# Kernel optimization log

Hardware: AMD Instinct MI355X
Metric: run time of the kernel (lower is better)

The kernel has to match this reference:

```python
import jax, jax.numpy as jnp
import numpy as np

B, S, D = 2, 2048, 2048
H = 16
DR = 64      # qk_rope_head_dim
DN = 64      # qk_nope_head_dim
DQK = DN + DR
DV = 128     # v_head_dim
QLR = 1536   # q_lora_rank
KVLR = 1024  # kv_lora_rank
THETA = 10000.0


def setup_inputs() -> dict:
    key = jax.random.key(0)
    ks = jax.random.split(key, 8)
    init = lambda k, shape: (jax.random.normal(k, shape, jnp.float32) * 0.02)
    x = jax.random.normal(ks[0], (B, S, D), jnp.float32)
    wq_a = init(ks[1], (QLR, D))
    q_norm_w = jnp.ones((QLR,), jnp.float32)
    wq_b = init(ks[2], (H * DQK, QLR))
    wkv_a = init(ks[3], (KVLR + DR, D))
    kv_norm_w = jnp.ones((KVLR,), jnp.float32)
    wkv_b = init(ks[4], (H * (DN + DV), KVLR))
    wo = init(ks[5], (D, H * DV))
    # rotary frequencies: angle[t, i] = t / theta^(2i/DR)  (complex freqs_cis = cos + i sin)
    inv_freq = 1.0 / (THETA ** (jnp.arange(0, DR, 2, dtype=jnp.float32) / DR))
    ang = jnp.arange(S, dtype=jnp.float32)[:, None] * inv_freq[None, :]  # [S, DR/2]
    freqs_cos, freqs_sin = jnp.cos(ang), jnp.sin(ang)
    # causal additive mask (large negative instead of -inf for grad safety)
    mask = jnp.where(jnp.triu(jnp.ones((S, S), bool), 1), -1e9, 0.0).astype(jnp.float32)
    return dict(x=x, wq_a=wq_a, q_norm_w=q_norm_w, wq_b=wq_b, wkv_a=wkv_a,
                kv_norm_w=kv_norm_w, wkv_b=wkv_b, wo=wo, mask=mask,
                freqs_cos=freqs_cos, freqs_sin=freqs_sin, start_pos=0)


def _rmsnorm(x, w, eps=1e-6):
    return x * jax.lax.rsqrt(jnp.mean(x * x, axis=-1, keepdims=True) + eps) * w


def _rope(x, cos, sin):
    # x: [B, S, h, d]; complex multiply on interleaved (even, odd) pairs
    x0, x1 = x[..., ::2], x[..., 1::2]
    c = cos[None, :, None, :]
    s = sin[None, :, None, :]
    return jnp.stack([x0 * c - x1 * s, x0 * s + x1 * c], axis=-1).reshape(x.shape)


def reference(x, wq_a, q_norm_w, wq_b, wkv_a, kv_norm_w, wkv_b, wo,
              mask, freqs_cos, freqs_sin, start_pos):
    # start_pos == 0 prefill: KV cache[:end_pos] equals current K/V.
    scale = DQK ** -0.5
    # low-rank Q: wq_b(q_norm(wq_a(x)))
    q = _rmsnorm(x @ wq_a.T, q_norm_w) @ wq_b.T
    q = q.reshape(B, S, H, DQK)
    q_nope, q_pe = q[..., :DN], q[..., DN:]
    q_pe = _rope(q_pe, freqs_cos, freqs_sin)
    # latent KV
    kv = x @ wkv_a.T                              # [B, S, KVLR + DR]
    c_kv, k_pe = kv[..., :KVLR], kv[..., KVLR:]
    k_pe = _rope(k_pe[:, :, None, :], freqs_cos, freqs_sin)   # [B, S, 1, DR]
    kv2 = (_rmsnorm(c_kv, kv_norm_w) @ wkv_b.T).reshape(B, S, H, DN + DV)
    k_nope, v = kv2[..., :DN], kv2[..., DN:]
    k = jnp.concatenate([k_nope, jnp.broadcast_to(k_pe, (B, S, H, DR))], axis=-1)
    qf = jnp.concatenate([q_nope, q_pe], axis=-1)             # [B, S, H, DQK]
    # scores laid out [B, S(q), H, T(k)] as in the torch code
    scores = jnp.einsum('bshd,bthd->bsht', qf, k) * scale + mask[None, :, None, :]
    attn = jax.nn.softmax(scores.astype(jnp.float32), axis=-1).astype(x.dtype)
    out = jnp.einsum('bsht,bthd->bshd', attn, v)              # [B, S, H, DV]
    return out.reshape(B, S, H * DV) @ wo.T
```

## Files before the change

kernel.cpp:

```cpp
#include <hip/hip_runtime.h>
#include <hip/hip_bf16.h>


using bf16 = __hip_bfloat16;
typedef __attribute__((ext_vector_type(8))) short bf16x8;
typedef __attribute__((ext_vector_type(4))) float f32x4;

#define S_ 2048
#define NEG_BIG (-1e30f)
#define LOG2E 1.4426950408889634f

static __device__ __forceinline__ f32x4 mfma16(bf16x8 a, bf16x8 b, f32x4 c) {
    return __builtin_amdgcn_mfma_f32_16x16x32_bf16(a, b, c, 0, 0, 0);
}

static __device__ __forceinline__ void gload_lds16(const bf16* g, bf16* l) {
    __builtin_amdgcn_global_load_lds(
        (const __attribute__((address_space(1))) void*)g,
        (__attribute__((address_space(3))) void*)l, 16, 0, 0);
}

__global__ __launch_bounds__(256) void f2b(const float* __restrict__ src,
                                           bf16* __restrict__ dst, int n4) {
    int i = blockIdx.x * 256 + threadIdx.x;
    if (i < n4) {
        float4 v = ((const float4*)src)[i];
        alignas(8) bf16 t[4];
        t[0] = (bf16)v.x; t[1] = (bf16)v.y; t[2] = (bf16)v.z; t[3] = (bf16)v.w;
        ((uint2*)dst)[i] = *(const uint2*)t;
    }
}

template <bool C_F32>
__global__ __launch_bounds__(256) void gemm_bt(const bf16* __restrict__ A,
                                               const bf16* __restrict__ Bw,
                                               void* __restrict__ Cv,
                                               int M, int N, int K,
                                               int lda, int ldb, int ldc) {
    __shared__ bf16 As[128 * 32];
    __shared__ bf16 Bs[128 * 32];
    const int tid = threadIdx.x;
    const int m0 = blockIdx.x * 128;
    const int n0 = blockIdx.y * 128;
    const int w = tid >> 6, lane = tid & 63, quad = lane >> 4, l15 = lane & 15;
    const int wr = (w >> 1) * 64, wc = (w & 1) * 64;

    f32x4 acc[4][4];
#pragma unroll
    for (int i = 0; i < 4; i++)
#pragma unroll
        for (int j = 0; j < 4; j++) acc[i][j] = (f32x4){0.f, 0.f, 0.f, 0.f};

    for (int k0 = 0; k0 < K; k0 += 32) {
        __syncthreads();
#pragma unroll
        for (int cc = 0; cc < 2; cc++) {
            int c = tid + cc * 256;
            int row = c >> 2;
            int chunk = (c & 3) ^ ((row >> 1) & 3);
            gload_lds16(A + (size_t)(m0 + row) * lda + k0 + chunk * 8, As + c * 8);
            gload_lds16(Bw + (size_t)(n0 + row) * ldb + k0 + chunk * 8, Bs + c * 8);
        }
        __syncthreads();
        bf16x8 af[4], bfr[4];
#pragma unroll
        for (int mi = 0; mi < 4; mi++) {
            int row = wr + mi * 16 + l15;
            int chunkE = quad ^ ((row >> 1) & 3);
            af[mi] = *(const bf16x8*)(&As[row * 32 + chunkE * 8]);
        }
#pragma unroll
        for (int ni = 0; ni < 4; ni++) {
            int row = wc + ni * 16 + l15;
            int chunkE = quad ^ ((row >> 1) & 3);
            bfr[ni] = *(const bf16x8*)(&Bs[row * 32 + chunkE * 8]);
        }
#pragma unroll
        for (int mi = 0; mi < 4; mi++)
#pragma unroll
            for (int ni = 0; ni < 4; ni++)
                acc[mi][ni] = mfma16(af[mi], bfr[ni], acc[mi][ni]);
    }

#pragma unroll
    for (int mi = 0; mi < 4; mi++) {
#pragma unroll
        for (int ni = 0; ni < 4; ni++) {
            int col = n0 + wc + ni * 16 + l15;
            if (col < N) {
#pragma unroll
                for (int r = 0; r < 4; r++) {
                    int row = m0 + wr + mi * 16 + quad * 4 + r;
                    if (C_F32) ((float*)Cv)[(size_t)row * ldc + col] = acc[mi][ni][r];
                    else       ((bf16*)Cv)[(size_t)row * ldc + col] = (bf16)acc[mi][ni][r];
                }
            }
        }
    }
}

__global__ void rmsnorm_ip(bf16* __restrict__ buf, const float* __restrict__ w,
                           int cols, int ld) {
    int row = blockIdx.x;
    bf16* p = buf + (size_t)row * ld;
    float ss = 0.f;
    for (int c = threadIdx.x; c < cols; c += 256) {
        float v = __bfloat162float(p[c]);
        ss += v * v;
    }
#pragma unroll
    for (int off = 32; off; off >>= 1) ss += __shfl_down(ss, off, 64);
    __shared__ float red[4];
    __shared__ float rnorm_s;
    if ((threadIdx.x & 63) == 0) red[threadIdx.x >> 6] = ss;
    __syncthreads();
    if (threadIdx.x == 0)
        rnorm_s = rsqrtf((red[0] + red[1] + red[2] + red[3]) / cols + 1e-6f);
    __syncthreads();
    float rn = rnorm_s;
    for (int c = threadIdx.x; c < cols; c += 256) {
        float v = __bfloat162float(p[c]);
        p[c] = (bf16)(v * rn * w[c]);
    }
}

__global__ void rope_k(const bf16* __restrict__ kvb, bf16* __restrict__ kpe,
                       const float* __restrict__ fc, const float* __restrict__ fs) {
    int id = blockIdx.x * 256 + threadIdx.x;
    int row = id >> 5, i = id & 31;
    int s = row & (S_ - 1);
    const bf16* p = kvb + (size_t)row * 1088 + 1024 + 2 * i;
    float x0 = __bfloat162float(p[0]), x1 = __bfloat162float(p[1]);
    float c = fc[s * 32 + i], sn = fs[s * 32 + i];
    bf16* q = kpe + (size_t)row * 64 + 2 * i;
    q[0] = (bf16)(x0 * c - x1 * sn);
    q[1] = (bf16)(x0 * sn + x1 * c);
}

__global__ void rope_q(bf16* __restrict__ qb, const float* __restrict__ fc,
                       const float* __restrict__ fs) {
    int id = blockIdx.x * 256 + threadIdx.x;
    int row = id >> 9, rest = id & 511, h = rest >> 5, i = rest & 31;
    int s = row & (S_ - 1);
    bf16* p = qb + (size_t)row * 2048 + h * 128 + 64 + 2 * i;
    float x0 = __bfloat162float(p[0]), x1 = __bfloat162float(p[1]);
    float c = fc[s * 32 + i], sn = fs[s * 32 + i];
    p[0] = (bf16)(x0 * c - x1 * sn);
    p[1] = (bf16)(x0 * sn + x1 * c);
}

__global__ __launch_bounds__(512) void attn_kernel(const bf16* __restrict__ Qg,
                                                   const bf16* __restrict__ KV2,
                                                   const bf16* __restrict__ KPE,
                                                   bf16* __restrict__ Og) {
    __shared__ bf16 Ks[64 * 128];
    __shared__ bf16 Vt[128 * 64];
    __shared__ bf16 Ps[8][16 * 64];
    const int tid = threadIdx.x;
    const int h = blockIdx.y;
    const int b = blockIdx.z;
    const int w = tid >> 6, lane = tid & 63, quad = lane >> 4, l15 = lane & 15;
    const int grp = w >> 2, wl = w & 3;
    const int jB = 31 - (int)blockIdx.x;
    const int q0 = (grp ? jB : (int)blockIdx.x) * 64;
    const int qrow = q0 + wl * 16 + l15;
    const float scl2 = 0.08838834764831845f * LOG2E;

    bf16x8 qf[4];
    {
        const bf16* qp = Qg + ((size_t)(b * S_) + qrow) * 2048 + h * 128 + quad * 8;
#pragma unroll
        for (int kk = 0; kk < 4; kk++) qf[kk] = *(const bf16x8*)(qp + kk * 32);
    }

    f32x4 acc_o[8];
#pragma unroll
    for (int j = 0; j < 8; j++) acc_o[j] = (f32x4){0.f, 0.f, 0.f, 0.f};
    float m_i = NEG_BIG, l_i = 0.f;
    const int s_base = q0 + wl * 16 + quad * 4;
    const int tend = jB * 64;

    const int dv0 = (tid >> 4) * 4;
    const int tv0 = (tid & 15) * 4;

    for (int t0 = 0; t0 <= tend; t0 += 64) {
        __syncthreads();
#pragma unroll
        for (int cc = 0; cc < 2; cc++) {
            int c = tid + cc * 512;
            int trow = c >> 4, chunk = c & 15;
            int col8 = chunk * 8;
            size_t grow = (size_t)(b * S_) + t0 + trow;
            int4 v;
            if (col8 < 64) v = *(const int4*)(KV2 + grow * 3072 + h * 192 + col8);
            else           v = *(const int4*)(KPE + grow * 64 + col8 - 64);
            int chunkE = chunk ^ (trow & 7);
            *(int4*)(&Ks[trow * 128 + chunkE * 8]) = v;
        }
        {
            size_t grow0 = (size_t)(b * S_) + t0 + tv0;
            alignas(16) bf16 va[4][4];
#pragma unroll
            for (int i = 0; i < 4; i++)
                *(uint2*)va[i] = *(const uint2*)(KV2 + (grow0 + i) * 3072 + h * 192 + 64 + dv0);
#pragma unroll
            for (int j = 0; j < 4; j++) {
                alignas(8) bf16 tmp[4] = {va[0][j], va[1][j], va[2][j], va[3][j]};
                int dv = dv0 + j;
                int cE = (tv0 >> 3) ^ (dv & 7);
                *(uint2*)(&Vt[dv * 64 + cE * 8 + (tv0 & 7)]) = *(uint2*)tmp;
            }
        }
        __syncthreads();
        if (t0 > q0) continue;

        f32x4 sc[4];
#pragma unroll
        for (int ni = 0; ni < 4; ni++) sc[ni] = (f32x4){0.f, 0.f, 0.f, 0.f};
#pragma unroll
        for (int kk = 0; kk < 4; kk++) {
#pragma unroll
            for (int ni = 0; ni < 4; ni++) {
                int trow = ni * 16 + l15;
                int chunkE = (kk * 4 + quad) ^ (trow & 7);
                bf16x8 kf = *(const bf16x8*)(&Ks[trow * 128 + chunkE * 8]);
                sc[ni] = mfma16(kf, qf[kk], sc[ni]);
            }
        }
        float xv[4][4];
        float pmax = NEG_BIG;
#pragma unroll
        for (int ni = 0; ni < 4; ni++) {
#pragma unroll
            for (int r = 0; r < 4; r++) {
                int t = t0 + ni * 16 + quad * 4 + r;
                float x = sc[ni][r] * scl2;
                if (t > qrow) x = NEG_BIG;
                xv[ni][r] = x;
                pmax = fmaxf(pmax, x);
            }
        }
        pmax = fmaxf(pmax, __shfl_xor(pmax, 16, 64));
        pmax = fmaxf(pmax, __shfl_xor(pmax, 32, 64));
        float mn = fmaxf(m_i, pmax);
        float alpha = exp2f(m_i - mn);
        m_i = mn;
        float rsum = 0.f;
#pragma unroll
        for (int ni = 0; ni < 4; ni++)
#pragma unroll
            for (int r = 0; r < 4; r++) {
                float e = exp2f(xv[ni][r] - mn);
                xv[ni][r] = e;
                rsum += e;
            }
        rsum += __shfl_xor(rsum, 16, 64);
        rsum += __shfl_xor(rsum, 32, 64);
        l_i = l_i * alpha + rsum;
        float ar[4];
#pragma unroll
        for (int r = 0; r < 4; r++) ar[r] = __shfl(alpha, quad * 4 + r, 64);
#pragma unroll
        for (int nj = 0; nj < 8; nj++)
#pragma unroll
            for (int r = 0; r < 4; r++) acc_o[nj][r] *= ar[r];

#pragma unroll
        for (int ni = 0; ni < 4; ni++) {
            int tb = ni * 16 + quad * 4;
            int cE = (tb >> 3) ^ (l15 & 7);
            alignas(8) bf16 tmp[4] = {(bf16)xv[ni][0], (bf16)xv[ni][1],
                                      (bf16)xv[ni][2], (bf16)xv[ni][3]};
            *(uint2*)(&Ps[w][l15 * 64 + cE * 8 + (tb & 7)]) = *(uint2*)tmp;
        }
#pragma unroll
        for (int kk2 = 0; kk2 < 2; kk2++) {
            int cEp = (kk2 * 4 + quad) ^ (l15 & 7);
            bf16x8 pf = *(const bf16x8*)(&Ps[w][l15 * 64 + cEp * 8]);
#pragma unroll
            for (int nj = 0; nj < 8; nj++) {
                int dv = nj * 16 + l15;
                int chunkE = (kk2 * 4 + quad) ^ (dv & 7);
                bf16x8 vf = *(const bf16x8*)(&Vt[dv * 64 + chunkE * 8]);
                acc_o[nj] = mfma16(pf, vf, acc_o[nj]);
            }
        }
    }
    float lr[4];
#pragma unroll
    for (int r = 0; r < 4; r++) lr[r] = __shfl(l_i, quad * 4 + r, 64);
#pragma unroll
    for (int nj = 0; nj < 8; nj++) {
        int col = h * 128 + nj * 16 + l15;
#pragma unroll
        for (int r = 0; r < 4; r++) {
            float v = acc_o[nj][r] / lr[r];
            Og[((size_t)(b * S_) + s_base + r) * 2048 + col] = (bf16)v;
        }
    }
}

extern "C" void kernel_launch(void* const* d_in, const int* in_sizes, int n_in,
                              void* d_out, int out_size, void* d_ws, size_t ws_size,
                              hipStream_t stream) {
    const float* x        = (const float*)d_in[0];
    const float* wq_a     = (const float*)d_in[1];
    const float* q_norm_w = (const float*)d_in[2];
    const float* wq_b     = (const float*)d_in[3];
    const float* wkv_a    = (const float*)d_in[4];
    const float* kv_norm_w= (const float*)d_in[5];
    const float* wkv_b    = (const float*)d_in[6];
    const float* wo       = (const float*)d_in[7];
    const float* fcos     = (const float*)d_in[9];
    const float* fsin     = (const float*)d_in[10];
    float* out = (float*)d_out;

    char* ws = (char*)d_ws;
    bf16* kv2   = (bf16*)(ws);
    bf16* kpe   = (bf16*)(ws + 25165824);
    bf16* kvb   = (bf16*)(ws + 25690112);
    bf16* qa    = (bf16*)(ws + 25690112);
    bf16* attno = (bf16*)(ws + 25690112);
    bf16* xb    = (bf16*)(ws + 43319296);
    bf16* wslot = (bf16*)(ws + 60096512);
    bf16* qbuf  = (bf16*)d_out;

    dim3 blk(256);
    f2b<<<8192, blk, 0, stream>>>(x, xb, 2097152);
    f2b<<<2176, blk, 0, stream>>>(wkv_a, wslot, 557056);
    gemm_bt<false><<<dim3(32, 9), blk, 0, stream>>>(xb, wslot, kvb, 4096, 1088, 2048, 2048, 2048, 1088);
    rope_k<<<512, blk, 0, stream>>>(kvb, kpe, fcos, fsin);
    rmsnorm_ip<<<4096, blk, 0, stream>>>(kvb, kv_norm_w, 1024, 1088);
    f2b<<<3072, blk, 0, stream>>>(wkv_b, wslot, 786432);
    gemm_bt<false><<<dim3(32, 24), blk, 0, stream>>>(kvb, wslot, kv2, 4096, 3072, 1024, 1088, 1024, 3072);
    f2b<<<3072, blk, 0, stream>>>(wq_a, wslot, 786432);
    gemm_bt<false><<<dim3(32, 12), blk, 0, stream>>>(xb, wslot, qa, 4096, 1536, 2048, 2048, 2048, 1536);
    rmsnorm_ip<<<4096, blk, 0, stream>>>(qa, q_norm_w, 1536, 1536);
    f2b<<<3072, blk, 0, stream>>>(wq_b, wslot, 786432);
    gemm_bt<false><<<dim3(32, 16), blk, 0, stream>>>(qa, wslot, qbuf, 4096, 2048, 1536, 1536, 1536, 2048);
    rope_q<<<8192, blk, 0, stream>>>(qbuf, fcos, fsin);
    attn_kernel<<<dim3(16, 16, 2), dim3(512), 0, stream>>>(qbuf, kv2, kpe, attno);
    f2b<<<4096, blk, 0, stream>>>(wo, wslot, 1048576);
    gemm_bt<true><<<dim3(32, 16), blk, 0, stream>>>(attno, wslot, out, 4096, 2048, 2048, 2048, 2048, 2048);
}
```

Before: 546.6 us.

## Double-buffer GEMM LDS, prefetch attention KV, fuse wq_a/wkv_a GEMMs, lazy rescale

The GEMM now double-buffers its LDS tiles, issuing the next K-slice's global-to-LDS loads before computing on the current one and using a single barrier per iteration. The attention kernel prefetches the next K/V tile into registers while the current tile is being computed, and skips the online-softmax rescale of the accumulator unless the running max grows by more than 8 in log2 units. The x@wkv_a and x@wq_a projections are merged into one wider GEMM writing a shared buffer, removing one pass over x. These changes add LDS use and register pressure, and the lazy rescale relies on a bounded exponent headroom.

```diff
diff --git a/kernel.cpp b/kernel.cpp
--- a/kernel.cpp
+++ b/kernel.cpp
@@ -37,8 +37,8 @@
                                                void* __restrict__ Cv,
                                                int M, int N, int K,
                                                int lda, int ldb, int ldc) {
-    __shared__ bf16 As[128 * 32];
-    __shared__ bf16 Bs[128 * 32];
+    __shared__ bf16 As[2][128 * 32];
+    __shared__ bf16 Bs[2][128 * 32];
     const int tid = threadIdx.x;
     const int m0 = blockIdx.x * 128;
     const int n0 = blockIdx.y * 128;
@@ -51,35 +51,44 @@
 #pragma unroll
         for (int j = 0; j < 4; j++) acc[i][j] = (f32x4){0.f, 0.f, 0.f, 0.f};
 
-    for (int k0 = 0; k0 < K; k0 += 32) {
-        __syncthreads();
+    auto stage = [&](int buf, int k0) {
 #pragma unroll
         for (int cc = 0; cc < 2; cc++) {
             int c = tid + cc * 256;
             int row = c >> 2;
             int chunk = (c & 3) ^ ((row >> 1) & 3);
-            gload_lds16(A + (size_t)(m0 + row) * lda + k0 + chunk * 8, As + c * 8);
-            gload_lds16(Bw + (size_t)(n0 + row) * ldb + k0 + chunk * 8, Bs + c * 8);
-        }
-        __syncthreads();
+            gload_lds16(A + (size_t)(m0 + row) * lda + k0 + chunk * 8, &As[buf][c * 8]);
+            gload_lds16(Bw + (size_t)(n0 + row) * ldb + k0 + chunk * 8, &Bs[buf][c * 8]);
+        }
+    };
+
+    stage(0, 0);
+    __syncthreads();
+    int cur = 0;
+    for (int k0 = 0; k0 < K; k0 += 32) {
+        if (k0 + 32 < K) stage(cur ^ 1, k0 + 32);
+        const bf16* Asc = As[cur];
+        const bf16* Bsc = Bs[cur];
         bf16x8 af[4], bfr[4];
 #pragma unroll
         for (int mi = 0; mi < 4; mi++) {
             int row = wr + mi * 16 + l15;
             int chunkE = quad ^ ((row >> 1) & 3);
-            af[mi] = *(const bf16x8*)(&As[row * 32 + chunkE * 8]);
+            af[mi] = *(const bf16x8*)(&Asc[row * 32 + chunkE * 8]);
         }
 #pragma unroll
         for (int ni = 0; ni < 4; ni++) {
             int row = wc + ni * 16 + l15;
             int chunkE = quad ^ ((row >> 1) & 3);
-            bfr[ni] = *(const bf16x8*)(&Bs[row * 32 + chunkE * 8]);
+            bfr[ni] = *(const bf16x8*)(&Bsc[row * 32 + chunkE * 8]);
         }
 #pragma unroll
         for (int mi = 0; mi < 4; mi++)
 #pragma unroll
             for (int ni = 0; ni < 4; ni++)
                 acc[mi][ni] = mfma16(af[mi], bfr[ni], acc[mi][ni]);
+        __syncthreads();
+        cur ^= 1;
     }
 
 #pragma unroll
@@ -124,12 +133,12 @@
     }
 }
 
-__global__ void rope_k(const bf16* __restrict__ kvb, bf16* __restrict__ kpe,
+__global__ void rope_k(const bf16* __restrict__ cq, bf16* __restrict__ kpe,
                        const float* __restrict__ fc, const float* __restrict__ fs) {
     int id = blockIdx.x * 256 + threadIdx.x;
     int row = id >> 5, i = id & 31;
     int s = row & (S_ - 1);
-    const bf16* p = kvb + (size_t)row * 1088 + 1024 + 2 * i;
+    const bf16* p = cq + (size_t)row * 2624 + 1024 + 2 * i;
     float x0 = __bfloat162float(p[0]), x1 = __bfloat162float(p[1]);
     float c = fc[s * 32 + i], sn = fs[s * 32 + i];
     bf16* q = kpe + (size_t)row * 64 + 2 * i;
@@ -183,34 +192,61 @@
     const int dv0 = (tid >> 4) * 4;
     const int tv0 = (tid & 15) * 4;
 
+    int4 kreg0, kreg1;
+    uint2 vreg0, vreg1, vreg2, vreg3;
+    auto loadKV = [&](int t0) {
+        {
+            int c = tid;
+            int trow = c >> 4, chunk = c & 15, col8 = chunk * 8;
+            size_t grow = (size_t)(b * S_) + t0 + trow;
+            kreg0 = (col8 < 64) ? *(const int4*)(KV2 + grow * 3072 + h * 192 + col8)
+                                : *(const int4*)(KPE + grow * 64 + col8 - 64);
+        }
+        {
+            int c = tid + 512;
+            int trow = c >> 4, chunk = c & 15, col8 = chunk * 8;
+            size_t grow = (size_t)(b * S_) + t0 + trow;
+            kreg1 = (col8 < 64) ? *(const int4*)(KV2 + grow * 3072 + h * 192 + col8)
+                                : *(const int4*)(KPE + grow * 64 + col8 - 64);
+        }
+        size_t grow0 = (size_t)(b * S_) + t0 + tv0;
+        const bf16* vb = KV2 + grow0 * 3072 + h * 192 + 64 + dv0;
+        vreg0 = *(const uint2*)(vb);
+        vreg1 = *(const uint2*)(vb + 3072);
+        vreg2 = *(const uint2*)(vb + 6144);
+        vreg3 = *(const uint2*)(vb + 9216);
+    };
+    auto writeKV = [&]() {
+        {
+            int c = tid;
+            int trow = c >> 4, chunk = c & 15;
+            int chunkE = chunk ^ (trow & 7);
+            *(int4*)(&Ks[trow * 128 + chunkE * 8]) = kreg0;
+        }
+        {
+            int c = tid + 512;
+            int trow = c >> 4, chunk = c & 15;
+            int chunkE = chunk ^ (trow & 7);
+            *(int4*)(&Ks[trow * 128 + chunkE * 8]) = kreg1;
+        }
+        const bf16* v0 = (const bf16*)&vreg0;
+        const bf16* v1 = (const bf16*)&vreg1;
+        const bf16* v2 = (const bf16*)&vreg2;
+        const bf16* v3 = (const bf16*)&vreg3;
+#pragma unroll
+        for (int j = 0; j < 4; j++) {
+            alignas(8) bf16 tmp[4] = {v0[j], v1[j], v2[j], v3[j]};
+            int dv = dv0 + j;
+            int cE = (tv0 >> 3) ^ (dv & 7);
+            *(uint2*)(&Vt[dv * 64 + cE * 8 + (tv0 & 7)]) = *(uint2*)tmp;
+        }
+    };
+
+    loadKV(0);
     for (int t0 = 0; t0 <= tend; t0 += 64) {
         __syncthreads();
-#pragma unroll
-        for (int cc = 0; cc < 2; cc++) {
-            int c = tid + cc * 512;
-            int trow = c >> 4, chunk = c & 15;
-            int col8 = chunk * 8;
-            size_t grow = (size_t)(b * S_) + t0 + trow;
-            int4 v;
-            if (col8 < 64) v = *(const int4*)(KV2 + grow * 3072 + h * 192 + col8);
-            else           v = *(const int4*)(KPE + grow * 64 + col8 - 64);
-            int chunkE = chunk ^ (trow & 7);
-            *(int4*)(&Ks[trow * 128 + chunkE * 8]) = v;
-        }
-        {
-            size_t grow0 = (size_t)(b * S_) + t0 + tv0;
-            alignas(16) bf16 va[4][4];
-#pragma unroll
-            for (int i = 0; i < 4; i++)
-                *(uint2*)va[i] = *(const uint2*)(KV2 + (grow0 + i) * 3072 + h * 192 + 64 + dv0);
-#pragma unroll
-            for (int j = 0; j < 4; j++) {
-                alignas(8) bf16 tmp[4] = {va[0][j], va[1][j], va[2][j], va[3][j]};
-                int dv = dv0 + j;
-                int cE = (tv0 >> 3) ^ (dv & 7);
-                *(uint2*)(&Vt[dv * 64 + cE * 8 + (tv0 & 7)]) = *(uint2*)tmp;
-            }
-        }
+        writeKV();
+        if (t0 + 64 <= tend) loadKV(t0 + 64);
         __syncthreads();
         if (t0 > q0) continue;
 
@@ -242,28 +278,31 @@
         }
         pmax = fmaxf(pmax, __shfl_xor(pmax, 16, 64));
         pmax = fmaxf(pmax, __shfl_xor(pmax, 32, 64));
-        float mn = fmaxf(m_i, pmax);
-        float alpha = exp2f(m_i - mn);
-        m_i = mn;
+        if (!__all(pmax - m_i <= 8.0f)) {
+            float mn = fmaxf(m_i, pmax);
+            float alpha = exp2f(m_i - mn);
+            m_i = mn;
+            l_i *= alpha;
+            float ar[4];
+#pragma unroll
+            for (int r = 0; r < 4; r++) ar[r] = __shfl(alpha, quad * 4 + r, 64);
+#pragma unroll
+            for (int nj = 0; nj < 8; nj++)
+#pragma unroll
+                for (int r = 0; r < 4; r++) acc_o[nj][r] *= ar[r];
+        }
         float rsum = 0.f;
 #pragma unroll
         for (int ni = 0; ni < 4; ni++)
 #pragma unroll
             for (int r = 0; r < 4; r++) {
-                float e = exp2f(xv[ni][r] - mn);
+                float e = exp2f(xv[ni][r] - m_i);
                 xv[ni][r] = e;
                 rsum += e;
             }
         rsum += __shfl_xor(rsum, 16, 64);
         rsum += __shfl_xor(rsum, 32, 64);
-        l_i = l_i * alpha + rsum;
-        float ar[4];
-#pragma unroll
-        for (int r = 0; r < 4; r++) ar[r] = __shfl(alpha, quad * 4 + r, 64);
-#pragma unroll
-        for (int nj = 0; nj < 8; nj++)
-#pragma unroll
-            for (int r = 0; r < 4; r++) acc_o[nj][r] *= ar[r];
+        l_i += rsum;
 
 #pragma unroll
         for (int ni = 0; ni < 4; ni++) {
@@ -318,26 +357,24 @@
     char* ws = (char*)d_ws;
     bf16* kv2   = (bf16*)(ws);
     bf16* kpe   = (bf16*)(ws + 25165824);
-    bf16* kvb   = (bf16*)(ws + 25690112);
-    bf16* qa    = (bf16*)(ws + 25690112);
-    bf16* attno = (bf16*)(ws + 25690112);
-    bf16* xb    = (bf16*)(ws + 43319296);
-    bf16* wslot = (bf16*)(ws + 60096512);
+    bf16* cq    = (bf16*)(ws + 25690112);
+    bf16* xb    = (bf16*)(ws + 47185920);
+    bf16* wslot = (bf16*)(ws + 63963136);
+    bf16* attno = cq;
     bf16* qbuf  = (bf16*)d_out;
 
     dim3 blk(256);
     f2b<<<8192, blk, 0, stream>>>(x, xb, 2097152);
     f2b<<<2176, blk, 0, stream>>>(wkv_a, wslot, 557056);
-    gemm_bt<false><<<dim3(32, 9), blk, 0, stream>>>(xb, wslot, kvb, 4096, 1088, 2048, 2048, 2048, 1088);
-    rope_k<<<512, blk, 0, stream>>>(kvb, kpe, fcos, fsin);
-    rmsnorm_ip<<<4096, blk, 0, stream>>>(kvb, kv_norm_w, 1024, 1088);
+    f2b<<<3072, blk, 0, stream>>>(wq_a, wslot + 1088 * 2048, 786432);
+    gemm_bt<false><<<dim3(32, 21), blk, 0, stream>>>(xb, wslot, cq, 4096, 2624, 2048, 2048, 2048, 2624);
+    rope_k<<<512, blk, 0, stream>>>(cq, kpe, fcos, fsin);
+    rmsnorm_ip<<<4096, blk, 0, stream>>>(cq, kv_norm_w, 1024, 2624);
     f2b<<<3072, blk, 0, stream>>>(wkv_b, wslot, 786432);
-    gemm_bt<false><<<dim3(32, 24), blk, 0, stream>>>(kvb, wslot, kv2, 4096, 3072, 1024, 1088, 1024, 3072);
-    f2b<<<3072, blk, 0, stream>>>(wq_a, wslot, 786432);
-    gemm_bt<false><<<dim3(32, 12), blk, 0, stream>>>(xb, wslot, qa, 4096, 1536, 2048, 2048, 2048, 1536);
-    rmsnorm_ip<<<4096, blk, 0, stream>>>(qa, q_norm_w, 1536, 1536);
+    gemm_bt<false><<<dim3(32, 24), blk, 0, stream>>>(cq, wslot, kv2, 4096, 3072, 1024, 2624, 1024, 3072);
+    rmsnorm_ip<<<4096, blk, 0, stream>>>(cq + 1088, q_norm_w, 1536, 2624);
     f2b<<<3072, blk, 0, stream>>>(wq_b, wslot, 786432);
-    gemm_bt<false><<<dim3(32, 16), blk, 0, stream>>>(qa, wslot, qbuf, 4096, 2048, 1536, 1536, 1536, 2048);
+    gemm_bt<false><<<dim3(32, 16), blk, 0, stream>>>(cq + 1088, wslot, qbuf, 4096, 2048, 1536, 2624, 1536, 2048);
     rope_q<<<8192, blk, 0, stream>>>(qbuf, fcos, fsin);
     attn_kernel<<<dim3(16, 16, 2), dim3(512), 0, stream>>>(qbuf, kv2, kpe, attno);
     f2b<<<4096, blk, 0, stream>>>(wo, wslot, 1048576);
```

Result: no change. 542.9 us (-0.7%).
